# Kernel tuning notes

Measured on AMD Instinct MI355X. Metric: run time of the kernel, lower is better.

The kernel has to match this reference:

```python
import jax, jax.numpy as jnp
import numpy as np

N, M, D = 8192, 8192, 512
TINY = jnp.finfo(jnp.float32).tiny


def setup_inputs() -> dict:
    key = jax.random.key(0)
    k1, k2 = jax.random.split(key)
    x = jax.random.normal(k1, (N, D), dtype=jnp.float32)
    x2 = jax.random.normal(k2, (M, D), dtype=jnp.float32)
    # flax self.param with ones initializer (pre-softplus raw params)
    amplitude_raw = jnp.ones((1,), dtype=jnp.float32)
    length_scale_raw = jnp.ones((D,), dtype=jnp.float32)
    return {"x": x, "x2": x2, "amplitude_raw": amplitude_raw,
            "length_scale_raw": length_scale_raw}


def reference(x, x2, amplitude_raw, length_scale_raw):
    # Parameter transforms exactly as in RBFKernelProvider.apply
    amplitude = jax.nn.softplus(amplitude_raw) + TINY          # (1,)
    length_scale = jax.nn.softplus(length_scale_raw) + TINY    # (D,)

    # rbf_kernel_fun: exp(-0.5 * sum(((x - x2)/l)^2)) * amp^2
    # GEMM rewrite of the squared scaled distance (avoids (N,M,D) intermediate):
    # ||xs_i - ys_j||^2 = ||xs_i||^2 + ||ys_j||^2 - 2 xs_i . ys_j
    xs = x / length_scale                                       # (N, D)
    ys = x2 / length_scale                                      # (M, D)
    x_sq = jnp.sum(xs * xs, axis=-1)                            # (N,)
    y_sq = jnp.sum(ys * ys, axis=-1)                            # (M,)
    cross = jnp.einsum('nd,md->nm', xs, ys)                     # (N, M) GEMM
    sq_dists = jnp.maximum(x_sq[:, None] + y_sq[None, :] - 2.0 * cross, 0.0)
    kernel_matrix = jnp.exp(-0.5 * sq_dists)                    # (N, M)
    return (amplitude ** 2) * kernel_matrix
```

## Files before the change

### kernel.cpp

```cpp
#include <hip/hip_runtime.h>

#define AS1 __attribute__((address_space(1)))
#define AS3 __attribute__((address_space(3)))

typedef __attribute__((ext_vector_type(4))) float f32x4;
typedef __attribute__((ext_vector_type(8))) int   i32x8;

static constexpr int Nn = 8192;
static constexpr int Mm = 8192;
static constexpr int Dd = 512;
static constexpr float TINY = 1.17549435082228751e-38f;

__device__ __forceinline__ float softplus_f(float x) {
    return fmaxf(x, 0.0f) + log1pf(expf(-fabsf(x)));
}

__device__ __forceinline__ void g2l16(const void* g, void* l) {
    __builtin_amdgcn_global_load_lds((const AS1 unsigned int*)g,
                                     (AS3 unsigned int*)l, 16, 0, 0);
}

__global__ __launch_bounds__(256) void scale_rows(
        const float* __restrict__ x, const float* __restrict__ x2,
        const float* __restrict__ ls_raw,
        unsigned char* __restrict__ xs, unsigned char* __restrict__ ys,
        float* __restrict__ x_sq, float* __restrict__ y_sq) {
    int wave = threadIdx.x >> 6, lane = threadIdx.x & 63;
    int row = blockIdx.x * 4 + wave;

    const float* src; unsigned char* dst; float* nrm; int r;
    if (row < Nn) {
        src = x  + (size_t)row * Dd; dst = xs + (size_t)row * 512;
        nrm = x_sq + row; r = row;
    } else {
        int m = row - Nn;
        src = x2 + (size_t)m * Dd;   dst = ys + (size_t)m * 512;
        nrm = y_sq + m; r = m;
    }

    float4 v0 = ((const float4*)src)[lane * 2];
    float4 v1 = ((const float4*)src)[lane * 2 + 1];
    float4 L0 = ((const float4*)ls_raw)[lane * 2];
    float4 L1 = ((const float4*)ls_raw)[lane * 2 + 1];

    float il[8] = {
        1.0f / (softplus_f(L0.x) + TINY), 1.0f / (softplus_f(L0.y) + TINY),
        1.0f / (softplus_f(L0.z) + TINY), 1.0f / (softplus_f(L0.w) + TINY),
        1.0f / (softplus_f(L1.x) + TINY), 1.0f / (softplus_f(L1.y) + TINY),
        1.0f / (softplus_f(L1.z) + TINY), 1.0f / (softplus_f(L1.w) + TINY) };
    float s[8] = { v0.x*il[0], v0.y*il[1], v0.z*il[2], v0.w*il[3],
                   v1.x*il[4], v1.y*il[5], v1.z*il[6], v1.w*il[7] };
    float sum = 0.0f;
#pragma unroll
    for (int i = 0; i < 8; ++i) sum += s[i] * s[i];

    int p0 = __builtin_amdgcn_cvt_pk_fp8_f32(s[0], s[1], 0, false);
    p0     = __builtin_amdgcn_cvt_pk_fp8_f32(s[2], s[3], p0, true);
    int p1 = __builtin_amdgcn_cvt_pk_fp8_f32(s[4], s[5], 0, false);
    p1     = __builtin_amdgcn_cvt_pk_fp8_f32(s[6], s[7], p1, true);

    int j    = lane >> 1;
    int phys = (j & ~7) | ((j & 7) ^ (r & 7));
    *(int2*)(dst + phys * 16 + (lane & 1) * 8) = make_int2(p0, p1);

#pragma unroll
    for (int off = 32; off > 0; off >>= 1) sum += __shfl_down(sum, off, 64);
    if (lane == 0) *nrm = sum;
}

__global__ __launch_bounds__(256) void gemm_rbf(
        const unsigned char* __restrict__ xs,
        const unsigned char* __restrict__ ys,
        const float* __restrict__ x_sq, const float* __restrict__ y_sq,
        const float* __restrict__ amp_raw, float* __restrict__ out) {

    __shared__ unsigned char sA[2][128 * 128];
    __shared__ unsigned char sB[2][128 * 128];

    const int tid  = threadIdx.x;
    const int wave = tid >> 6, lane = tid & 63;
    const int wy = wave >> 1, wx = wave & 1;
    const int lane15 = lane & 15, quad = lane >> 4;
    const int srow = lane >> 3, schunk = lane & 7;

    const unsigned lin = blockIdx.y * 64u + blockIdx.x;
    const unsigned swz = (lin & 7u) * 512u + (lin >> 3);
    const size_t rowBase = (size_t)(swz >> 6) * 128;
    const size_t colBase = (size_t)(swz & 63u) * 128;

    auto stage = [&](int buf, int kt) {
        const size_t kOff = (size_t)kt * 128;
#pragma unroll
        for (int t = 0; t < 4; ++t) {
            int issue = wave * 4 + t;
            int rit = issue * 8 + srow;
            g2l16(xs + (rowBase + rit) * 512 + kOff + schunk * 16,
                  sA[buf] + issue * 1024);
            g2l16(ys + (colBase + rit) * 512 + kOff + schunk * 16,
                  sB[buf] + issue * 1024);
        }
    };

    float xq[4][4], yq[4];
#pragma unroll
    for (int ty = 0; ty < 4; ++ty) {
        const size_t r0 = rowBase + wy * 64 + ty * 16 + quad * 4;
#pragma unroll
        for (int i = 0; i < 4; ++i) xq[ty][i] = x_sq[r0 + i];
    }
#pragma unroll
    for (int tx = 0; tx < 4; ++tx)
        yq[tx] = y_sq[colBase + wx * 64 + tx * 16 + lane15];
    float a = softplus_f(amp_raw[0]) + TINY;
    const float amp2 = a * a;

    f32x4 acc[4][4] = {};

    stage(0, 0);
    __syncthreads();

#pragma unroll
    for (int kt = 0; kt < 4; ++kt) {
        const int cur = kt & 1;
        if (kt < 3) stage(cur ^ 1, kt + 1);

        i32x8 bF[4];
#pragma unroll
        for (int tx = 0; tx < 4; ++tx) {
            int rr = wx * 64 + tx * 16 + lane15;
            int x7 = rr & 7;
            int p0 = (quad * 2 + 0) ^ x7, p1 = (quad * 2 + 1) ^ x7;
            int4 lo = *(const int4*)(sB[cur] + rr * 128 + p0 * 16);
            int4 hi = *(const int4*)(sB[cur] + rr * 128 + p1 * 16);
            i32x8 f; f[0]=lo.x; f[1]=lo.y; f[2]=lo.z; f[3]=lo.w;
                     f[4]=hi.x; f[5]=hi.y; f[6]=hi.z; f[7]=hi.w;
            bF[tx] = f;
        }
#pragma unroll
        for (int ty = 0; ty < 4; ++ty) {
            int rr = wy * 64 + ty * 16 + lane15;
            int x7 = rr & 7;
            int p0 = (quad * 2 + 0) ^ x7, p1 = (quad * 2 + 1) ^ x7;
            int4 lo = *(const int4*)(sA[cur] + rr * 128 + p0 * 16);
            int4 hi = *(const int4*)(sA[cur] + rr * 128 + p1 * 16);
            i32x8 aF; aF[0]=lo.x; aF[1]=lo.y; aF[2]=lo.z; aF[3]=lo.w;
                      aF[4]=hi.x; aF[5]=hi.y; aF[6]=hi.z; aF[7]=hi.w;
#pragma unroll
            for (int tx = 0; tx < 4; ++tx)
                acc[ty][tx] = __builtin_amdgcn_mfma_scale_f32_16x16x128_f8f6f4(
                    aF, bF[tx], acc[ty][tx],
                    0 , 0 ,
                    0, 0x7F7F7F7F,
                    0, 0x7F7F7F7F);
        }
        __syncthreads();
    }

#pragma unroll
    for (int ty = 0; ty < 4; ++ty) {
        const size_t r0 = rowBase + wy * 64 + ty * 16 + quad * 4;
#pragma unroll
        for (int tx = 0; tx < 4; ++tx) {
            const size_t gc = colBase + wx * 64 + tx * 16 + lane15;
            float* o = out + r0 * (size_t)Mm + gc;
#pragma unroll
            for (int reg = 0; reg < 4; ++reg) {
                float sq = fmaxf(xq[ty][reg] + yq[tx] - 2.0f * acc[ty][tx][reg],
                                 0.0f);
                __builtin_nontemporal_store(amp2 * __expf(-0.5f * sq),
                                            o + (size_t)reg * Mm);
            }
        }
    }
}

__global__ __launch_bounds__(256) void rbf_fallback(
        const float* __restrict__ x, const float* __restrict__ x2,
        const float* __restrict__ amp_raw, const float* __restrict__ ls_raw,
        float* __restrict__ out) {
    __shared__ float il[Dd];
    __shared__ float sX[16 * Dd];
    __shared__ float sY[16 * Dd];
    int tid = threadIdx.x;
    for (int i = tid; i < Dd; i += 256)
        il[i] = 1.0f / (softplus_f(ls_raw[i]) + TINY);
    __syncthreads();
    int bR = blockIdx.y * 16, bC = blockIdx.x * 16;
    for (int i = tid; i < 16 * Dd; i += 256) {
        int r = i >> 9, c = i & (Dd - 1);
        sX[i] = x [(size_t)(bR + r) * Dd + c] * il[c];
        sY[i] = x2[(size_t)(bC + r) * Dd + c] * il[c];
    }
    __syncthreads();
    float a = softplus_f(amp_raw[0]) + TINY;
    float amp2 = a * a;
    int r = tid >> 4, c = tid & 15;
    float sq = 0.0f;
    for (int d = 0; d < Dd; ++d) {
        float df = sX[r * Dd + d] - sY[c * Dd + d];
        sq += df * df;
    }
    out[(size_t)(bR + r) * Mm + (bC + c)] = amp2 * __expf(-0.5f * sq);
}

extern "C" void kernel_launch(void* const* d_in, const int* in_sizes, int n_in,
                              void* d_out, int out_size, void* d_ws, size_t ws_size,
                              hipStream_t stream) {
    const float* x       = (const float*)d_in[0];
    const float* x2      = (const float*)d_in[1];
    const float* amp_raw = (const float*)d_in[2];
    const float* ls_raw  = (const float*)d_in[3];
    float* out = (float*)d_out;

    const size_t OFF_XSQ = 0;
    const size_t OFF_YSQ = OFF_XSQ + 8192 * 4;
    const size_t OFF_XS  = OFF_YSQ + 8192 * 4;
    const size_t OFF_YS  = OFF_XS + (size_t)Nn * Dd;
    const size_t NEED    = OFF_YS + (size_t)Mm * Dd;

    if (ws_size < NEED) {
        dim3 g(Mm / 16, Nn / 16);
        rbf_fallback<<<g, 256, 0, stream>>>(x, x2, amp_raw, ls_raw, out);
        return;
    }

    char* ws = (char*)d_ws;
    float* x_sq = (float*)(ws + OFF_XSQ);
    float* y_sq = (float*)(ws + OFF_YSQ);
    unsigned char* xs = (unsigned char*)(ws + OFF_XS);
    unsigned char* ys = (unsigned char*)(ws + OFF_YS);

    scale_rows<<<(Nn + Mm) / 4, 256, 0, stream>>>(x, x2, ls_raw, xs, ys, x_sq, y_sq);
    dim3 g(Mm / 128, Nn / 128);
    gemm_rbf<<<g, 256, 0, stream>>>(xs, ys, x_sq, y_sq, amp_raw, out);
}
```

Baseline: 343.7 us.

## Stage RBF epilogue through LDS for 16-byte row stores and fold exp into exp2

The fp32 epilogue now goes through shared memory. Each warp writes its exponentiated tile into a padded LDS buffer, and rows are then read back and stored as contiguous 16-byte nontemporal vectors instead of scattered 4-byte stores. The exponent is rewritten as a single exp2 of an FMA with the amplitude folded in as a log term. To free LDS for the staging buffer, the K-loop drops double buffering and becomes single-buffered with two barriers per step, which exposes global load latency. The epilogue also adds extra barriers.

```diff
diff --git a/kernel.cpp b/kernel.cpp
--- a/kernel.cpp
+++ b/kernel.cpp
@@ -13,6 +13,14 @@
 
 __device__ __forceinline__ float softplus_f(float x) {
     return fmaxf(x, 0.0f) + log1pf(expf(-fabsf(x)));
+}
+
+__device__ __forceinline__ float fast_exp2(float x) {
+#if __has_builtin(__builtin_amdgcn_exp2f)
+    return __builtin_amdgcn_exp2f(x);
+#else
+    return exp2f(x);
+#endif
 }
 
 __device__ __forceinline__ void g2l16(const void* g, void* l) {
@@ -74,8 +82,10 @@
         const float* __restrict__ x_sq, const float* __restrict__ y_sq,
         const float* __restrict__ amp_raw, float* __restrict__ out) {
 
-    __shared__ unsigned char sA[2][128 * 128];
-    __shared__ unsigned char sB[2][128 * 128];
+    __shared__ unsigned char smem[32768];
+    unsigned char* sA = smem;
+    unsigned char* sB = smem + 16384;
+    float* sT = (float*)smem;
 
     const int tid  = threadIdx.x;
     const int wave = tid >> 6, lane = tid & 63;
@@ -88,41 +98,33 @@
     const size_t rowBase = (size_t)(swz >> 6) * 128;
     const size_t colBase = (size_t)(swz & 63u) * 128;
 
-    auto stage = [&](int buf, int kt) {
+    float xq[4][4], yq[4];
+#pragma unroll
+    for (int ty = 0; ty < 4; ++ty) {
+        const size_t r0 = rowBase + wy * 64 + ty * 16 + quad * 4;
+#pragma unroll
+        for (int i = 0; i < 4; ++i) xq[ty][i] = x_sq[r0 + i];
+    }
+#pragma unroll
+    for (int tx = 0; tx < 4; ++tx)
+        yq[tx] = y_sq[colBase + wx * 64 + tx * 16 + lane15];
+    float a = softplus_f(amp_raw[0]) + TINY;
+
+    f32x4 acc[4][4] = {};
+
+    for (int kt = 0; kt < 4; ++kt) {
+        __syncthreads();
         const size_t kOff = (size_t)kt * 128;
 #pragma unroll
         for (int t = 0; t < 4; ++t) {
             int issue = wave * 4 + t;
             int rit = issue * 8 + srow;
             g2l16(xs + (rowBase + rit) * 512 + kOff + schunk * 16,
-                  sA[buf] + issue * 1024);
+                  sA + issue * 1024);
             g2l16(ys + (colBase + rit) * 512 + kOff + schunk * 16,
-                  sB[buf] + issue * 1024);
-        }
-    };
-
-    float xq[4][4], yq[4];
-#pragma unroll
-    for (int ty = 0; ty < 4; ++ty) {
-        const size_t r0 = rowBase + wy * 64 + ty * 16 + quad * 4;
-#pragma unroll
-        for (int i = 0; i < 4; ++i) xq[ty][i] = x_sq[r0 + i];
-    }
-#pragma unroll
-    for (int tx = 0; tx < 4; ++tx)
-        yq[tx] = y_sq[colBase + wx * 64 + tx * 16 + lane15];
-    float a = softplus_f(amp_raw[0]) + TINY;
-    const float amp2 = a * a;
-
-    f32x4 acc[4][4] = {};
-
-    stage(0, 0);
-    __syncthreads();
-
-#pragma unroll
-    for (int kt = 0; kt < 4; ++kt) {
-        const int cur = kt & 1;
-        if (kt < 3) stage(cur ^ 1, kt + 1);
+                  sB + issue * 1024);
+        }
+        __syncthreads();
 
         i32x8 bF[4];
 #pragma unroll
@@ -130,8 +132,8 @@
             int rr = wx * 64 + tx * 16 + lane15;
             int x7 = rr & 7;
             int p0 = (quad * 2 + 0) ^ x7, p1 = (quad * 2 + 1) ^ x7;
-            int4 lo = *(const int4*)(sB[cur] + rr * 128 + p0 * 16);
-            int4 hi = *(const int4*)(sB[cur] + rr * 128 + p1 * 16);
+            int4 lo = *(const int4*)(sB + rr * 128 + p0 * 16);
+            int4 hi = *(const int4*)(sB + rr * 128 + p1 * 16);
             i32x8 f; f[0]=lo.x; f[1]=lo.y; f[2]=lo.z; f[3]=lo.w;
                      f[4]=hi.x; f[5]=hi.y; f[6]=hi.z; f[7]=hi.w;
             bF[tx] = f;
@@ -141,8 +143,8 @@
             int rr = wy * 64 + ty * 16 + lane15;
             int x7 = rr & 7;
             int p0 = (quad * 2 + 0) ^ x7, p1 = (quad * 2 + 1) ^ x7;
-            int4 lo = *(const int4*)(sA[cur] + rr * 128 + p0 * 16);
-            int4 hi = *(const int4*)(sA[cur] + rr * 128 + p1 * 16);
+            int4 lo = *(const int4*)(sA + rr * 128 + p0 * 16);
+            int4 hi = *(const int4*)(sA + rr * 128 + p1 * 16);
             i32x8 aF; aF[0]=lo.x; aF[1]=lo.y; aF[2]=lo.z; aF[3]=lo.w;
                       aF[4]=hi.x; aF[5]=hi.y; aF[6]=hi.z; aF[7]=hi.w;
 #pragma unroll
@@ -153,24 +155,42 @@
                     0, 0x7F7F7F7F,
                     0, 0x7F7F7F7F);
         }
-        __syncthreads();
-    }
-
+    }
+
+    const float L2E = 1.44269504088896340736f;
+    const float la  = 2.0f * __log2f(a);
+    float hx[4][4], hy[4];
+#pragma unroll
+    for (int ty = 0; ty < 4; ++ty)
+#pragma unroll
+        for (int i = 0; i < 4; ++i) hx[ty][i] = -0.5f * L2E * xq[ty][i];
+#pragma unroll
+    for (int tx = 0; tx < 4; ++tx) hy[tx] = -0.5f * L2E * yq[tx];
+
+    __syncthreads();
 #pragma unroll
     for (int ty = 0; ty < 4; ++ty) {
-        const size_t r0 = rowBase + wy * 64 + ty * 16 + quad * 4;
 #pragma unroll
         for (int tx = 0; tx < 4; ++tx) {
-            const size_t gc = colBase + wx * 64 + tx * 16 + lane15;
-            float* o = out + r0 * (size_t)Mm + gc;
 #pragma unroll
             for (int reg = 0; reg < 4; ++reg) {
-                float sq = fmaxf(xq[ty][reg] + yq[tx] - 2.0f * acc[ty][tx][reg],
-                                 0.0f);
-                __builtin_nontemporal_store(amp2 * __expf(-0.5f * sq),
-                                            o + (size_t)reg * Mm);
+                float t = fminf(fmaf(acc[ty][tx][reg], L2E,
+                                     hx[ty][reg] + hy[tx]), 0.0f);
+                sT[(wy * 16 + quad * 4 + reg) * 132 +
+                   (wx * 64 + tx * 16 + lane15)] = fast_exp2(t + la);
             }
         }
+        __syncthreads();
+#pragma unroll
+        for (int i = 0; i < 4; ++i) {
+            int l    = wave * 8 + i * 2 + (lane >> 5);
+            int grow = (l >> 4) * 64 + ty * 16 + (l & 15);
+            int col  = (lane & 31) * 4;
+            f32x4 v  = *(const f32x4*)(sT + l * 132 + col);
+            __builtin_nontemporal_store(v,
+                (f32x4*)(out + (rowBase + grow) * (size_t)Mm + colBase + col));
+        }
+        __syncthreads();
     }
 }
 
```

New measurement: 331.3 us. 3.6% less time.

## Switch to 32x32x64 FP8 MFMA with K=64 double-buffered stages and exp2 epilogue

Applied to the files above, without the earlier changes.

Replaces the 16x16x128 scaled FP8 MFMA tiles with 32x32x64 tiles, each wave holding 2x2 accumulators of 16 floats. The LDS staging now uses 64-wide K slices over 8 iterations, with a new XOR swizzle applied at load time, so the scale kernel writes rows unswizzled. Synchronisation is now explicit vmcnt waits plus raw barriers. The block-to-tile mapping is remapped per XCD, and launch bounds request 4 blocks per CU. The epilogue folds -0.5*log2e and log(amp^2) into a single fma followed by a hardware exp2, and loads x_sq as float4. The aim is fewer LDS fragment reads per MFMA, better overlap and occupancy, and cheaper epilogue math. The cost is more barriers per K and a more fragile swizzle and wait-count scheme.

```diff
diff --git a/kernel.cpp b/kernel.cpp
--- a/kernel.cpp
+++ b/kernel.cpp
@@ -3,8 +3,9 @@
 #define AS1 __attribute__((address_space(1)))
 #define AS3 __attribute__((address_space(3)))
 
-typedef __attribute__((ext_vector_type(4))) float f32x4;
-typedef __attribute__((ext_vector_type(8))) int   i32x8;
+typedef __attribute__((ext_vector_type(4)))  float f32x4;
+typedef __attribute__((ext_vector_type(16))) float f32x16;
+typedef __attribute__((ext_vector_type(8)))  int   i32x8;
 
 static constexpr int Nn = 8192;
 static constexpr int Mm = 8192;
@@ -13,6 +14,14 @@
 
 __device__ __forceinline__ float softplus_f(float x) {
     return fmaxf(x, 0.0f) + log1pf(expf(-fabsf(x)));
+}
+
+__device__ __forceinline__ float fast_exp2(float x) {
+#if __has_builtin(__builtin_amdgcn_exp2f)
+    return __builtin_amdgcn_exp2f(x);
+#else
+    return exp2f(x);
+#endif
 }
 
 __device__ __forceinline__ void g2l16(const void* g, void* l) {
@@ -28,14 +37,14 @@
     int wave = threadIdx.x >> 6, lane = threadIdx.x & 63;
     int row = blockIdx.x * 4 + wave;
 
-    const float* src; unsigned char* dst; float* nrm; int r;
+    const float* src; unsigned char* dst; float* nrm;
     if (row < Nn) {
         src = x  + (size_t)row * Dd; dst = xs + (size_t)row * 512;
-        nrm = x_sq + row; r = row;
+        nrm = x_sq + row;
     } else {
         int m = row - Nn;
         src = x2 + (size_t)m * Dd;   dst = ys + (size_t)m * 512;
-        nrm = y_sq + m; r = m;
+        nrm = y_sq + m;
     }
 
     float4 v0 = ((const float4*)src)[lane * 2];
@@ -59,116 +68,124 @@
     int p1 = __builtin_amdgcn_cvt_pk_fp8_f32(s[4], s[5], 0, false);
     p1     = __builtin_amdgcn_cvt_pk_fp8_f32(s[6], s[7], p1, true);
 
-    int j    = lane >> 1;
-    int phys = (j & ~7) | ((j & 7) ^ (r & 7));
-    *(int2*)(dst + phys * 16 + (lane & 1) * 8) = make_int2(p0, p1);
+    *(int2*)(dst + lane * 8) = make_int2(p0, p1);
 
 #pragma unroll
     for (int off = 32; off > 0; off >>= 1) sum += __shfl_down(sum, off, 64);
     if (lane == 0) *nrm = sum;
 }
 
-__global__ __launch_bounds__(256) void gemm_rbf(
+__global__ __launch_bounds__(256, 4) void gemm_rbf(
         const unsigned char* __restrict__ xs,
         const unsigned char* __restrict__ ys,
         const float* __restrict__ x_sq, const float* __restrict__ y_sq,
         const float* __restrict__ amp_raw, float* __restrict__ out) {
 
-    __shared__ unsigned char sA[2][128 * 128];
-    __shared__ unsigned char sB[2][128 * 128];
+    __shared__ unsigned char smem[32768];
 
     const int tid  = threadIdx.x;
     const int wave = tid >> 6, lane = tid & 63;
     const int wy = wave >> 1, wx = wave & 1;
-    const int lane15 = lane & 15, quad = lane >> 4;
-    const int srow = lane >> 3, schunk = lane & 7;
+    const int lane31 = lane & 31, half = lane >> 5;
 
     const unsigned lin = blockIdx.y * 64u + blockIdx.x;
-    const unsigned swz = (lin & 7u) * 512u + (lin >> 3);
-    const size_t rowBase = (size_t)(swz >> 6) * 128;
-    const size_t colBase = (size_t)(swz & 63u) * 128;
-
+    const unsigned xcd = lin & 7u;
+    const unsigned t   = lin >> 3;
+    const size_t colBase = (size_t)(xcd * 8u + (t & 7u)) * 128;
+    const size_t rowBase = (size_t)(t >> 3) * 128;
+
+    const int sR0 = wave * 8 + (lane >> 3);
+    const int sp  = lane & 7;
     auto stage = [&](int buf, int kt) {
-        const size_t kOff = (size_t)kt * 128;
-#pragma unroll
-        for (int t = 0; t < 4; ++t) {
-            int issue = wave * 4 + t;
-            int rit = issue * 8 + srow;
-            g2l16(xs + (rowBase + rit) * 512 + kOff + schunk * 16,
-                  sA[buf] + issue * 1024);
-            g2l16(ys + (colBase + rit) * 512 + kOff + schunk * 16,
-                  sB[buf] + issue * 1024);
+#pragma unroll
+        for (int tt = 0; tt < 4; ++tt) {
+            const int i = tt & 1;
+            const int R = i * 32 + sR0;
+            const int c = sp ^ (R & 7);
+            const int r = 2 * R + (c >> 2);
+            const size_t gofs = (size_t)r * 512 + (size_t)kt * 64 + (c & 3) * 16;
+            const unsigned char* g = (tt < 2) ? xs + rowBase * 512 + gofs
+                                              : ys + colBase * 512 + gofs;
+            g2l16(g, smem + buf * 16384 + (tt >> 1) * 8192 + i * 4096
+                         + wave * 1024);
         }
     };
 
-    float xq[4][4], yq[4];
-#pragma unroll
-    for (int ty = 0; ty < 4; ++ty) {
-        const size_t r0 = rowBase + wy * 64 + ty * 16 + quad * 4;
-#pragma unroll
-        for (int i = 0; i < 4; ++i) xq[ty][i] = x_sq[r0 + i];
-    }
-#pragma unroll
-    for (int tx = 0; tx < 4; ++tx)
-        yq[tx] = y_sq[colBase + wx * 64 + tx * 16 + lane15];
-    float a = softplus_f(amp_raw[0]) + TINY;
-    const float amp2 = a * a;
-
-    f32x4 acc[4][4] = {};
-
-    stage(0, 0);
-    __syncthreads();
-
-#pragma unroll
-    for (int kt = 0; kt < 4; ++kt) {
-        const int cur = kt & 1;
-        if (kt < 3) stage(cur ^ 1, kt + 1);
-
-        i32x8 bF[4];
-#pragma unroll
-        for (int tx = 0; tx < 4; ++tx) {
-            int rr = wx * 64 + tx * 16 + lane15;
-            int x7 = rr & 7;
-            int p0 = (quad * 2 + 0) ^ x7, p1 = (quad * 2 + 1) ^ x7;
-            int4 lo = *(const int4*)(sB[cur] + rr * 128 + p0 * 16);
-            int4 hi = *(const int4*)(sB[cur] + rr * 128 + p1 * 16);
-            i32x8 f; f[0]=lo.x; f[1]=lo.y; f[2]=lo.z; f[3]=lo.w;
-                     f[4]=hi.x; f[5]=hi.y; f[6]=hi.z; f[7]=hi.w;
-            bF[tx] = f;
-        }
-#pragma unroll
-        for (int ty = 0; ty < 4; ++ty) {
-            int rr = wy * 64 + ty * 16 + lane15;
-            int x7 = rr & 7;
-            int p0 = (quad * 2 + 0) ^ x7, p1 = (quad * 2 + 1) ^ x7;
-            int4 lo = *(const int4*)(sA[cur] + rr * 128 + p0 * 16);
-            int4 hi = *(const int4*)(sA[cur] + rr * 128 + p1 * 16);
-            i32x8 aF; aF[0]=lo.x; aF[1]=lo.y; aF[2]=lo.z; aF[3]=lo.w;
-                      aF[4]=hi.x; aF[5]=hi.y; aF[6]=hi.z; aF[7]=hi.w;
-#pragma unroll
-            for (int tx = 0; tx < 4; ++tx)
-                acc[ty][tx] = __builtin_amdgcn_mfma_scale_f32_16x16x128_f8f6f4(
+    auto ldfrag = [&](const unsigned char* base, int rr) {
+        const int R  = rr >> 1;
+        const int x7 = R & 7;
+        const int c0 = (rr & 1) * 4 + 2 * half;
+        const int4 lo = *(const int4*)(base + R * 128 + (c0 ^ x7) * 16);
+        const int4 hi = *(const int4*)(base + R * 128 + ((c0 + 1) ^ x7) * 16);
+        i32x8 f; f[0]=lo.x; f[1]=lo.y; f[2]=lo.z; f[3]=lo.w;
+                 f[4]=hi.x; f[5]=hi.y; f[6]=hi.z; f[7]=hi.w;
+        return f;
+    };
+
+    f32x16 acc[2][2] = {};
+
+    auto compute = [&](int buf) {
+        const unsigned char* A = smem + buf * 16384;
+        const unsigned char* B = A + 8192;
+        i32x8 bF[2];
+#pragma unroll
+        for (int tx = 0; tx < 2; ++tx)
+            bF[tx] = ldfrag(B, wx * 64 + tx * 32 + lane31);
+#pragma unroll
+        for (int ty = 0; ty < 2; ++ty) {
+            i32x8 aF = ldfrag(A, wy * 64 + ty * 32 + lane31);
+#pragma unroll
+            for (int tx = 0; tx < 2; ++tx)
+                acc[ty][tx] = __builtin_amdgcn_mfma_scale_f32_32x32x64_f8f6f4(
                     aF, bF[tx], acc[ty][tx],
                     0 , 0 ,
                     0, 0x7F7F7F7F,
                     0, 0x7F7F7F7F);
         }
-        __syncthreads();
-    }
-
-#pragma unroll
-    for (int ty = 0; ty < 4; ++ty) {
-        const size_t r0 = rowBase + wy * 64 + ty * 16 + quad * 4;
-#pragma unroll
-        for (int tx = 0; tx < 4; ++tx) {
-            const size_t gc = colBase + wx * 64 + tx * 16 + lane15;
-            float* o = out + r0 * (size_t)Mm + gc;
-#pragma unroll
-            for (int reg = 0; reg < 4; ++reg) {
-                float sq = fmaxf(xq[ty][reg] + yq[tx] - 2.0f * acc[ty][tx][reg],
-                                 0.0f);
-                __builtin_nontemporal_store(amp2 * __expf(-0.5f * sq),
-                                            o + (size_t)reg * Mm);
+    };
+
+    stage(0, 0);
+#pragma unroll
+    for (int kt = 0; kt < 8; ++kt) {
+        if (kt < 7) {
+            stage((kt + 1) & 1, kt + 1);
+            asm volatile("s_waitcnt vmcnt(4)" ::: "memory");
+        } else {
+            asm volatile("s_waitcnt vmcnt(0)" ::: "memory");
+        }
+        __builtin_amdgcn_s_barrier();
+        __builtin_amdgcn_sched_barrier(0);
+        compute(kt & 1);
+        __builtin_amdgcn_s_barrier();
+    }
+
+    const float L2E = 1.44269504088896340736f;
+    const float a   = softplus_f(amp_raw[0]) + TINY;
+    const float la  = 2.0f * __log2f(a);
+    float yq[2];
+#pragma unroll
+    for (int tx = 0; tx < 2; ++tx)
+        yq[tx] = -0.5f * L2E * y_sq[colBase + wx * 64 + tx * 32 + lane31];
+
+#pragma unroll
+    for (int ty = 0; ty < 2; ++ty) {
+        const size_t r0 = rowBase + wy * 64 + ty * 32 + 4 * half;
+#pragma unroll
+        for (int g = 0; g < 4; ++g) {
+            float4 xv = *(const float4*)(x_sq + r0 + 8 * g);
+            float hx[4] = { -0.5f * L2E * xv.x, -0.5f * L2E * xv.y,
+                            -0.5f * L2E * xv.z, -0.5f * L2E * xv.w };
+#pragma unroll
+            for (int tx = 0; tx < 2; ++tx) {
+                const size_t gc = colBase + wx * 64 + tx * 32 + lane31;
+#pragma unroll
+                for (int j = 0; j < 4; ++j) {
+                    const int reg = g * 4 + j;
+                    float t2 = fminf(fmaf(acc[ty][tx][reg], L2E,
+                                          hx[j] + yq[tx]), 0.0f);
+                    __builtin_nontemporal_store(fast_exp2(t2 + la),
+                        out + (r0 + 8 * g + j) * (size_t)Mm + gc);
+                }
             }
         }
     }
```

New measurement: 310.0 us (median of 2 runs). 9.8% less time.
